# Kernel tuning notes

Measured on AMD Instinct MI355X. Metric: run time of the kernel, lower is better.

The kernel has to match this reference:

```python
import jax, jax.numpy as jnp
import numpy as np

B, L, P, NH = 16384, 64, 2, 128
T = L // P          # number of patches (GRU steps)
NOUT = 1 << P       # softmax over 2**p possible patches


def setup_inputs() -> dict:
    key = jax.random.key(0)
    ks = jax.random.split(key, 10)
    s_in = 1.0 / np.sqrt(NH)
    x = jax.random.randint(ks[0], (B, L, 1), 0, 2).astype(jnp.float32)
    return {
        "x": x,
        # GRU params, torch layout: gates ordered (r, z, n)
        "w_ih": jax.random.normal(ks[1], (3 * NH, P), jnp.float32) * s_in,
        "w_hh": jax.random.normal(ks[2], (3 * NH, NH), jnp.float32) * s_in,
        "b_ih": jax.random.normal(ks[3], (3 * NH,), jnp.float32) * s_in,
        "b_hh": jax.random.normal(ks[4], (3 * NH,), jnp.float32) * s_in,
        # MLP head: Linear(Nh,Nh) -> ReLU -> Linear(Nh, 2**p) -> Softmax
        "w1": jax.random.normal(ks[5], (NH, NH), jnp.float32) * s_in,
        "b1": jax.random.normal(ks[6], (NH,), jnp.float32) * s_in,
        "w2": jax.random.normal(ks[7], (NOUT, NH), jnp.float32) * s_in,
        "b2": jax.random.normal(ks[8], (NOUT,), jnp.float32) * s_in,
    }


def _gru_mlp_logp(x, w_ih, w_hh, b_ih, b_hh, w1, b1, w2, b2):
    b = x.shape[0]
    patches = x.reshape(b, T, P)                       # Patch1D.forward
    # shift right by one patch (teacher forcing input), first step is zeros
    data = jnp.concatenate([jnp.zeros((b, 1, P), x.dtype), patches[:, :-1]], axis=1)
    # precompute all input-side gate projections: [B,T,3*Nh]
    xi = jnp.einsum('btp,gp->btg', data, w_ih) + b_ih

    def step(h, xi_t):
        gi_r, gi_z, gi_n = jnp.split(xi_t, 3, axis=-1)
        gh = h @ w_hh.T + b_hh
        gh_r, gh_z, gh_n = jnp.split(gh, 3, axis=-1)
        r = jax.nn.sigmoid(gi_r + gh_r)
        z = jax.nn.sigmoid(gi_z + gh_z)
        n = jnp.tanh(gi_n + r * gh_n)
        h_new = (1.0 - z) * n + z * h
        return h_new, h_new

    h0 = jnp.zeros((b, NH), x.dtype)
    _, hs = jax.lax.scan(step, h0, jnp.swapaxes(xi, 0, 1))  # [T,B,Nh]
    hs = jnp.swapaxes(hs, 0, 1)                              # [B,T,Nh]

    hid = jax.nn.relu(hs @ w1.T + b1)
    probs = jax.nn.softmax(hid @ w2.T + b2, axis=-1)         # [B,T,2**p]

    # genpatch2onehot: binary-encode each patch, little-endian (bit i -> 2**i)
    weights = (1 << jnp.arange(P)).astype(jnp.float32)
    idx = jnp.sum(patches * weights, axis=-1).astype(jnp.int32)  # [B,T]
    total = jnp.take_along_axis(probs, idx[..., None], axis=-1)[..., 0]
    return jnp.sum(jnp.log(total), axis=1)                   # [B]


def reference(x, w_ih, w_hh, b_ih, b_hh, w1, b1, w2, b2):
    return _gru_mlp_logp(x, w_ih, w_hh, b_ih, b_hh, w1, b1, w2, b2)
```

## Files before the change

kernel.cpp:

```cpp
#include <hip/hip_runtime.h>
#include <hip/hip_bf16.h>


#define NSTEP 32
#define BT    32
#define BLK   256

using s8v = __attribute__((ext_vector_type(8))) short;
using f4v = __attribute__((ext_vector_type(4))) float;

#define L2E 1.4426950408889634f
#define LN2 0.6931471805599453f

__device__ __forceinline__ unsigned short f2bf(float f) {
  __hip_bfloat16 h = __float2bfloat16(f);
  return __builtin_bit_cast(unsigned short, h);
}
__device__ __forceinline__ unsigned pkbf2(float a, float b) {
  return (unsigned)f2bf(a) | ((unsigned)f2bf(b) << 16);
}
__device__ __forceinline__ s8v pack8(float4 u, float4 v) {
  s8v a;
  a[0]=(short)f2bf(u.x); a[1]=(short)f2bf(u.y); a[2]=(short)f2bf(u.z); a[3]=(short)f2bf(u.w);
  a[4]=(short)f2bf(v.x); a[5]=(short)f2bf(v.y); a[6]=(short)f2bf(v.z); a[7]=(short)f2bf(v.w);
  return a;
}
__device__ __forceinline__ f4v mfma16(s8v a, s8v b, f4v c) {
  return __builtin_amdgcn_mfma_f32_16x16x32_bf16(a, b, c, 0, 0, 0);
}
__device__ __forceinline__ float sigm(float x) {
  return __builtin_amdgcn_rcpf(1.f + __builtin_amdgcn_exp2f(-L2E * x));
}
__device__ __forceinline__ float tanhc(float x) {
  return __builtin_fmaf(2.f, __builtin_amdgcn_rcpf(1.f + __builtin_amdgcn_exp2f((-2.f*L2E) * x)), -1.f);
}

__global__ __launch_bounds__(BLK, 2) void prnn_kernel(
    const float* __restrict__ x, const float* __restrict__ w_ih,
    const float* __restrict__ w_hh, const float* __restrict__ b_ih,
    const float* __restrict__ b_hh, const float* __restrict__ w1,
    const float* __restrict__ b1, const float* __restrict__ w2,
    const float* __restrict__ b2, float* __restrict__ out) {

  __shared__ __align__(16) unsigned char lds_whhn[8*4*64*16];
  __shared__ __align__(16) unsigned char lds_h[4*2*64*16];
  __shared__ __align__(16) unsigned char lds_hid[2*4*2*64*16];
  __shared__ __align__(16) unsigned char lds_w2f[4*64*16];
  __shared__ __align__(16) float lds_xrz[64*4*4];
  __shared__ __align__(16) float lds_xn[32*4*4];
  __shared__ unsigned lds_idx[32*8];
  __shared__ float lds_lp[4][32];

  const int tid = threadIdx.x;
  const int bbase = blockIdx.x * BT;
  const int lane = tid & 63;
  const int lg = lane >> 4, ln = lane & 15;
  const int js = __builtin_amdgcn_readfirstlane(tid >> 6);

  {
    int b = tid >> 3, ch = tid & 7;
    const float* xp = x + (size_t)(bbase + b) * 64 + ch * 8;
    float4 v0 = *(const float4*)xp, v1 = *(const float4*)(xp + 4);
    unsigned pk = ((v0.x!=0.f?1u:0u) | (v0.y!=0.f?2u:0u))
               | (((v0.z!=0.f?1u:0u) | (v0.w!=0.f?2u:0u)) << 8)
               | (((v1.x!=0.f?1u:0u) | (v1.y!=0.f?2u:0u)) << 16)
               | (((v1.z!=0.f?1u:0u) | (v1.w!=0.f?2u:0u)) << 24);
    lds_idx[b*8 + ch] = pk;
  }
  {
    int j = tid;
    float base = b_ih[j] + b_hh[j];
    float wa = w_ih[2*j], wb = w_ih[2*j+1];
    int q = j >> 2, e = j & 3;
    #pragma unroll
    for (int v = 0; v < 4; ++v)
      lds_xrz[(q*4+v)*4 + e] = base + ((v&1) ? wa : 0.f) + ((v&2) ? wb : 0.f);
    if (tid < 128) {
      int j2 = 256 + tid;
      float bn = b_ih[j2];
      float wan = w_ih[2*j2], wbn = w_ih[2*j2+1];
      int qn = tid >> 2, en = tid & 3;
      #pragma unroll
      for (int v = 0; v < 4; ++v)
        lds_xn[(qn*4+v)*4 + en] = bn + ((v&1) ? wan : 0.f) + ((v&2) ? wbn : 0.f);
    }
  }
  #pragma unroll
  for (int it = 0; it < 8; ++it) {
    int i = tid + it * 256;
    int mt = i >> 8, ks = (i >> 6) & 3, l = i & 63;
    int lgg = l >> 4, lnn = l & 15;
    const float* src = w_hh + (256 + 16*mt + lnn) * 128 + ks*32 + lgg*8;
    s8v fr = pack8(*(const float4*)src, *(const float4*)(src + 4));
    *(s8v*)(lds_whhn + ((mt*4 + ks)*64 + l) * 16) = fr;
  }
  {
    int ks = tid >> 6, l = tid & 63;
    int lgg = l >> 4, lnn = l & 15;
    s8v fr;
    #pragma unroll
    for (int e = 0; e < 8; ++e) fr[e] = (short)0;
    if (lnn < 4) {
      const float* src = w2 + lnn * 128 + ks*32 + lgg*8;
      fr = pack8(*(const float4*)src, *(const float4*)(src + 4));
    }
    *(s8v*)(lds_w2f + (ks*64 + l) * 16) = fr;
  }

  s8v Ar[2][4], Az[2][4], wA1[2][4];
  f4v bhn2[2], b1f[2], b2r;
  #pragma unroll
  for (int p = 0; p < 2; ++p) {
    int row = 32*js + 16*p + ln;
    #pragma unroll
    for (int ks = 0; ks < 4; ++ks) {
      const float* s0 = w_hh + row * 128 + ks*32 + lg*8;
      Ar[p][ks] = pack8(*(const float4*)s0, *(const float4*)(s0 + 4));
      const float* s1 = w_hh + (128 + row) * 128 + ks*32 + lg*8;
      Az[p][ks] = pack8(*(const float4*)s1, *(const float4*)(s1 + 4));
      const float* s2 = w1 + row * 128 + ks*32 + lg*8;
      wA1[p][ks] = pack8(*(const float4*)s2, *(const float4*)(s2 + 4));
    }
    int jr = 32*js + 16*p + 4*lg;
    bhn2[p] = *(const f4v*)(b_hh + 256 + jr);
    b1f[p]  = *(const f4v*)(b1 + jr);
  }
  if (lg == 0) b2r = *(const f4v*)b2;
  else { b2r[0]=0.f; b2r[1]=0.f; b2r[2]=0.f; b2r[3]=0.f; }

  __syncthreads();

  unsigned pk0a=0, pk0b=0, pk1a=0, pk1b=0;
  #pragma unroll
  for (int w8 = 0; w8 < 4; ++w8) {
    unsigned u = lds_idx[ln*8 + w8];
    pk0a |= (((u&3u) | ((u>>6)&0xCu) | ((u>>12)&0x30u) | ((u>>18)&0xC0u)) << (8*w8));
    unsigned u2 = lds_idx[(16+ln)*8 + w8];
    pk1a |= (((u2&3u) | ((u2>>6)&0xCu) | ((u2>>12)&0x30u) | ((u2>>18)&0xC0u)) << (8*w8));
  }
  #pragma unroll
  for (int w8 = 4; w8 < 8; ++w8) {
    unsigned u = lds_idx[ln*8 + w8];
    pk0b |= (((u&3u) | ((u>>6)&0xCu) | ((u>>12)&0x30u) | ((u>>18)&0xC0u)) << (8*(w8-4)));
    unsigned u2 = lds_idx[(16+ln)*8 + w8];
    pk1b |= (((u2&3u) | ((u2>>6)&0xCu) | ((u2>>12)&0x30u) | ((u2>>18)&0xC0u)) << (8*(w8-4)));
  }

  const f4v* XRZ = (const f4v*)lds_xrz;
  const f4v* XN  = (const f4v*)lds_xn;

  s8v Bf[4][2];
  #pragma unroll
  for (int ks = 0; ks < 4; ++ks)
    #pragma unroll
    for (int nt = 0; nt < 2; ++nt)
      #pragma unroll
      for (int e = 0; e < 8; ++e) Bf[ks][nt][e] = (short)0;
  f4v hfr[2][2];
  #pragma unroll
  for (int p = 0; p < 2; ++p)
    #pragma unroll
    for (int nt = 0; nt < 2; ++nt) { hfr[p][nt][0]=0.f; hfr[p][nt][1]=0.f; hfr[p][nt][2]=0.f; hfr[p][nt][3]=0.f; }
  float lp0 = 0.f, lp1 = 0.f;
  int pv0 = 0, pv1 = 0;

  for (int tb = 0; tb < NSTEP; tb += 4) {
    #pragma unroll
    for (int k = 0; k < 4; ++k) {
      const int t = tb + k;
      uint2 hwv[2][2];
      #pragma unroll
      for (int nt = 0; nt < 2; ++nt) {
        const int var = nt ? pv1 : pv0;
        f4v aR[2], aZ[2], aN[2], xnv[2];
        #pragma unroll
        for (int p = 0; p < 2; ++p) {
          const int q = 8*js + 4*p + lg;
          aR[p]  = XRZ[(q     )*4 + var];
          aZ[p]  = XRZ[(q + 32)*4 + var];
          xnv[p] = XN [(q     )*4 + var];
          aN[p]  = bhn2[p];
        }
        #pragma unroll
        for (int ks = 0; ks < 4; ++ks) {
          s8v An0 = *(const s8v*)(lds_whhn + (((2*js+0)*4 + ks)*64 + lane)*16);
          s8v An1 = *(const s8v*)(lds_whhn + (((2*js+1)*4 + ks)*64 + lane)*16);
          aR[0] = mfma16(Ar[0][ks], Bf[ks][nt], aR[0]);
          aR[1] = mfma16(Ar[1][ks], Bf[ks][nt], aR[1]);
          aZ[0] = mfma16(Az[0][ks], Bf[ks][nt], aZ[0]);
          aZ[1] = mfma16(Az[1][ks], Bf[ks][nt], aZ[1]);
          aN[0] = mfma16(An0,       Bf[ks][nt], aN[0]);
          aN[1] = mfma16(An1,       Bf[ks][nt], aN[1]);
        }
        #pragma unroll
        for (int p = 0; p < 2; ++p) {
          f4v hn;
          #pragma unroll
          for (int r = 0; r < 4; ++r) {
            float R  = sigm(aR[p][r]);
            float Z  = sigm(aZ[p][r]);
            float Ng = tanhc(__builtin_fmaf(R, aN[p][r], xnv[p][r]));
            hn[r] = __builtin_fmaf(Z, hfr[p][nt][r] - Ng, Ng);
          }
          hfr[p][nt] = hn;
          hwv[p][nt].x = pkbf2(hn[0], hn[1]);
          hwv[p][nt].y = pkbf2(hn[2], hn[3]);
        }
      }
      #pragma unroll
      for (int p = 0; p < 2; ++p) {
        const int lgp = (2*p + (lg >> 1)) & 3;
        #pragma unroll
        for (int nt = 0; nt < 2; ++nt)
          *(uint2*)(lds_h + (((js*2 + nt)*64) + lgp*16 + ln)*16 + 8*(lg & 1)) = hwv[p][nt];
      }
      __syncthreads();
      #pragma unroll
      for (int ks = 0; ks < 4; ++ks)
        #pragma unroll
        for (int nt = 0; nt < 2; ++nt)
          Bf[ks][nt] = *(const s8v*)(lds_h + ((ks*2 + nt)*64 + lane)*16);
      f4v hc[2][2];
      #pragma unroll
      for (int p = 0; p < 2; ++p) { hc[p][0] = b1f[p]; hc[p][1] = b1f[p]; }
      #pragma unroll
      for (int ks = 0; ks < 4; ++ks)
        #pragma unroll
        for (int p = 0; p < 2; ++p) {
          hc[p][0] = mfma16(wA1[p][ks], Bf[ks][0], hc[p][0]);
          hc[p][1] = mfma16(wA1[p][ks], Bf[ks][1], hc[p][1]);
        }
      #pragma unroll
      for (int p = 0; p < 2; ++p) {
        const int lgp = (2*p + (lg >> 1)) & 3;
        #pragma unroll
        for (int nt = 0; nt < 2; ++nt) {
          uint2 wv;
          wv.x = pkbf2(fmaxf(hc[p][nt][0], 0.f), fmaxf(hc[p][nt][1], 0.f));
          wv.y = pkbf2(fmaxf(hc[p][nt][2], 0.f), fmaxf(hc[p][nt][3], 0.f));
          *(uint2*)(lds_hid + (k&1)*8192 + ((js*2 + nt)*64 + lgp*16 + ln)*16 + 8*(lg & 1)) = wv;
        }
      }
      __syncthreads();
      const unsigned pc0 = (t & 16) ? pk0b : pk0a;
      const unsigned pc1 = (t & 16) ? pk1b : pk1a;
      const int sh  = (2*t) & 31;
      const int ic0 = (pc0 >> sh) & 3;
      const int ic1 = (pc1 >> sh) & 3;
      if (js == k) {
        f4v la0 = b2r, la1 = b2r;
        #pragma unroll
        for (int ks = 0; ks < 4; ++ks) {
          s8v W2f = *(const s8v*)(lds_w2f + (ks*64 + lane)*16);
          s8v Bh0 = *(const s8v*)(lds_hid + (k&1)*8192 + ((ks*2 + 0)*64 + lane)*16);
          s8v Bh1 = *(const s8v*)(lds_hid + (k&1)*8192 + ((ks*2 + 1)*64 + lane)*16);
          la0 = mfma16(W2f, Bh0, la0);
          la1 = mfma16(W2f, Bh1, la1);
        }
        if (lg == 0) {
          {
            float l0=la0[0], l1=la0[1], l2=la0[2], l3=la0[3];
            float m = fmaxf(fmaxf(l0, l1), fmaxf(l2, l3));
            float s = __builtin_amdgcn_exp2f((l0-m)*L2E) + __builtin_amdgcn_exp2f((l1-m)*L2E)
                    + __builtin_amdgcn_exp2f((l2-m)*L2E) + __builtin_amdgcn_exp2f((l3-m)*L2E);
            float sel = (ic0 == 0) ? l0 : (ic0 == 1) ? l1 : (ic0 == 2) ? l2 : l3;
            lp0 += (sel - m) - __builtin_amdgcn_logf(s) * LN2;
          }
          {
            float l0=la1[0], l1=la1[1], l2=la1[2], l3=la1[3];
            float m = fmaxf(fmaxf(l0, l1), fmaxf(l2, l3));
            float s = __builtin_amdgcn_exp2f((l0-m)*L2E) + __builtin_amdgcn_exp2f((l1-m)*L2E)
                    + __builtin_amdgcn_exp2f((l2-m)*L2E) + __builtin_amdgcn_exp2f((l3-m)*L2E);
            float sel = (ic1 == 0) ? l0 : (ic1 == 1) ? l1 : (ic1 == 2) ? l2 : l3;
            lp1 += (sel - m) - __builtin_amdgcn_logf(s) * LN2;
          }
        }
      }
      pv0 = ic0; pv1 = ic1;
    }
  }

  if (lg == 0) { lds_lp[js][ln] = lp0; lds_lp[js][16 + ln] = lp1; }
  __syncthreads();
  if (tid < 32) {
    float s = lds_lp[0][tid] + lds_lp[1][tid] + lds_lp[2][tid] + lds_lp[3][tid];
    out[bbase + tid] = s;
  }
}

extern "C" void kernel_launch(void* const* d_in, const int* in_sizes, int n_in,
                              void* d_out, int out_size, void* d_ws, size_t ws_size,
                              hipStream_t stream) {
  const float* x    = (const float*)d_in[0];
  const float* w_ih = (const float*)d_in[1];
  const float* w_hh = (const float*)d_in[2];
  const float* b_ih = (const float*)d_in[3];
  const float* b_hh = (const float*)d_in[4];
  const float* w1   = (const float*)d_in[5];
  const float* b1   = (const float*)d_in[6];
  const float* w2   = (const float*)d_in[7];
  const float* b2   = (const float*)d_in[8];
  float* out = (float*)d_out;
  int B = in_sizes[0] / 64;
  int grid = B / BT;
  prnn_kernel<<<grid, BLK, 0, stream>>>(x, w_ih, w_hh, b_ih, b_hh, w1, b1, w2, b2, out);
}
```

Before: 105.4 us.

## Split GRU hidden rows across eight waves and move W1 to LDS

```diff
diff --git a/kernel.cpp b/kernel.cpp
--- a/kernel.cpp
+++ b/kernel.cpp
@@ -4,7 +4,7 @@
 
 #define NSTEP 32
 #define BT    32
-#define BLK   256
+#define BLK   512
 
 using s8v = __attribute__((ext_vector_type(8))) short;
 using f4v = __attribute__((ext_vector_type(4))) float;
@@ -35,29 +35,31 @@
   return __builtin_fmaf(2.f, __builtin_amdgcn_rcpf(1.f + __builtin_amdgcn_exp2f((-2.f*L2E) * x)), -1.f);
 }
 
-__global__ __launch_bounds__(BLK, 2) void prnn_kernel(
+__global__ __launch_bounds__(BLK, 4) void prnn_kernel(
     const float* __restrict__ x, const float* __restrict__ w_ih,
     const float* __restrict__ w_hh, const float* __restrict__ b_ih,
     const float* __restrict__ b_hh, const float* __restrict__ w1,
     const float* __restrict__ b1, const float* __restrict__ w2,
     const float* __restrict__ b2, float* __restrict__ out) {
 
-  __shared__ __align__(16) unsigned char lds_whhn[8*4*64*16];
   __shared__ __align__(16) unsigned char lds_h[4*2*64*16];
-  __shared__ __align__(16) unsigned char lds_hid[2*4*2*64*16];
+  __shared__ __align__(16) unsigned char lds_hid[4*2*64*16];
+  __shared__ __align__(16) unsigned char lds_wA1[8*4*64*16];
   __shared__ __align__(16) unsigned char lds_w2f[4*64*16];
   __shared__ __align__(16) float lds_xrz[64*4*4];
   __shared__ __align__(16) float lds_xn[32*4*4];
+  __shared__ __align__(16) float lds_bb[256];
+  __shared__ __align__(16) float lds_b2[4];
   __shared__ unsigned lds_idx[32*8];
-  __shared__ float lds_lp[4][32];
+  __shared__ float lds_lp[8][32];
 
   const int tid = threadIdx.x;
   const int bbase = blockIdx.x * BT;
   const int lane = tid & 63;
   const int lg = lane >> 4, ln = lane & 15;
-  const int js = __builtin_amdgcn_readfirstlane(tid >> 6);
-
-  {
+  const int w = __builtin_amdgcn_readfirstlane(tid >> 6);
+
+  if (tid < 256) {
     int b = tid >> 3, ch = tid & 7;
     const float* xp = x + (size_t)(bbase + b) * 64 + ch * 8;
     float4 v0 = *(const float4*)xp, v1 = *(const float4*)(xp + 4);
@@ -67,7 +69,7 @@
                | (((v1.z!=0.f?1u:0u) | (v1.w!=0.f?2u:0u)) << 24);
     lds_idx[b*8 + ch] = pk;
   }
-  {
+  if (tid < 256) {
     int j = tid;
     float base = b_ih[j] + b_hh[j];
     float wa = w_ih[2*j], wb = w_ih[2*j+1];
@@ -75,58 +77,51 @@
     #pragma unroll
     for (int v = 0; v < 4; ++v)
       lds_xrz[(q*4+v)*4 + e] = base + ((v&1) ? wa : 0.f) + ((v&2) ? wb : 0.f);
-    if (tid < 128) {
-      int j2 = 256 + tid;
-      float bn = b_ih[j2];
-      float wan = w_ih[2*j2], wbn = w_ih[2*j2+1];
-      int qn = tid >> 2, en = tid & 3;
-      #pragma unroll
-      for (int v = 0; v < 4; ++v)
-        lds_xn[(qn*4+v)*4 + en] = bn + ((v&1) ? wan : 0.f) + ((v&2) ? wbn : 0.f);
-    }
-  }
-  #pragma unroll
-  for (int it = 0; it < 8; ++it) {
-    int i = tid + it * 256;
+  }
+  if (tid < 128) {
+    int j2 = 256 + tid;
+    float bn = b_ih[j2];
+    float wan = w_ih[2*j2], wbn = w_ih[2*j2+1];
+    int qn = tid >> 2, en = tid & 3;
+    #pragma unroll
+    for (int v = 0; v < 4; ++v)
+      lds_xn[(qn*4+v)*4 + en] = bn + ((v&1) ? wan : 0.f) + ((v&2) ? wbn : 0.f);
+  }
+  if (tid < 128) lds_bb[tid] = b_hh[256 + tid];
+  else if (tid < 256) lds_bb[tid] = b1[tid - 128];
+  if (tid < 4) lds_b2[tid] = b2[tid];
+  #pragma unroll
+  for (int it = 0; it < 4; ++it) {
+    int i = tid + it * BLK;
     int mt = i >> 8, ks = (i >> 6) & 3, l = i & 63;
-    int lgg = l >> 4, lnn = l & 15;
-    const float* src = w_hh + (256 + 16*mt + lnn) * 128 + ks*32 + lgg*8;
-    s8v fr = pack8(*(const float4*)src, *(const float4*)(src + 4));
-    *(s8v*)(lds_whhn + ((mt*4 + ks)*64 + l) * 16) = fr;
-  }
-  {
+    const float* src = w1 + (16*mt + (l & 15)) * 128 + ks*32 + (l >> 4)*8;
+    *(s8v*)(lds_wA1 + ((mt*4 + ks)*64 + l)*16) = pack8(*(const float4*)src, *(const float4*)(src+4));
+  }
+  if (tid < 256) {
     int ks = tid >> 6, l = tid & 63;
-    int lgg = l >> 4, lnn = l & 15;
     s8v fr;
     #pragma unroll
     for (int e = 0; e < 8; ++e) fr[e] = (short)0;
-    if (lnn < 4) {
-      const float* src = w2 + lnn * 128 + ks*32 + lgg*8;
+    if ((l & 15) < 4) {
+      const float* src = w2 + (l & 15) * 128 + ks*32 + (l >> 4)*8;
       fr = pack8(*(const float4*)src, *(const float4*)(src + 4));
     }
-    *(s8v*)(lds_w2f + (ks*64 + l) * 16) = fr;
-  }
-
-  s8v Ar[2][4], Az[2][4], wA1[2][4];
-  f4v bhn2[2], b1f[2], b2r;
-  #pragma unroll
-  for (int p = 0; p < 2; ++p) {
-    int row = 32*js + 16*p + ln;
+    *(s8v*)(lds_w2f + (ks*64 + l)*16) = fr;
+  }
+
+  s8v Ar[4], Az[4], An[4];
+  {
+    const int row = 16*w + ln;
     #pragma unroll
     for (int ks = 0; ks < 4; ++ks) {
-      const float* s0 = w_hh + row * 128 + ks*32 + lg*8;
-      Ar[p][ks] = pack8(*(const float4*)s0, *(const float4*)(s0 + 4));
-      const float* s1 = w_hh + (128 + row) * 128 + ks*32 + lg*8;
-      Az[p][ks] = pack8(*(const float4*)s1, *(const float4*)(s1 + 4));
-      const float* s2 = w1 + row * 128 + ks*32 + lg*8;
-      wA1[p][ks] = pack8(*(const float4*)s2, *(const float4*)(s2 + 4));
+      const float* s0 = w_hh + row*128 + ks*32 + lg*8;
+      Ar[ks] = pack8(*(const float4*)s0, *(const float4*)(s0 + 4));
+      const float* s1 = s0 + 128*128;
+      Az[ks] = pack8(*(const float4*)s1, *(const float4*)(s1 + 4));
+      const float* s2 = s0 + 256*128;
+      An[ks] = pack8(*(const float4*)s2, *(const float4*)(s2 + 4));
     }
-    int jr = 32*js + 16*p + 4*lg;
-    bhn2[p] = *(const f4v*)(b_hh + 256 + jr);
-    b1f[p]  = *(const f4v*)(b1 + jr);
-  }
-  if (lg == 0) b2r = *(const f4v*)b2;
-  else { b2r[0]=0.f; b2r[1]=0.f; b2r[2]=0.f; b2r[3]=0.f; }
+  }
 
   __syncthreads();
 
@@ -146,8 +141,8 @@
     pk1b |= (((u2&3u) | ((u2>>6)&0xCu) | ((u2>>12)&0x30u) | ((u2>>18)&0xC0u)) << (8*(w8-4)));
   }
 
-  const f4v* XRZ = (const f4v*)lds_xrz;
-  const f4v* XN  = (const f4v*)lds_xn;
+  const unsigned wroff = (unsigned)((((w>>1)*128) + 16*(2*(w&1) + (lg>>1)) + ln)*16 + 8*(lg&1));
+  const int q = 4*w + lg;
 
   s8v Bf[4][2];
   #pragma unroll
@@ -156,63 +151,45 @@
     for (int nt = 0; nt < 2; ++nt)
       #pragma unroll
       for (int e = 0; e < 8; ++e) Bf[ks][nt][e] = (short)0;
-  f4v hfr[2][2];
-  #pragma unroll
-  for (int p = 0; p < 2; ++p)
-    #pragma unroll
-    for (int nt = 0; nt < 2; ++nt) { hfr[p][nt][0]=0.f; hfr[p][nt][1]=0.f; hfr[p][nt][2]=0.f; hfr[p][nt][3]=0.f; }
+  f4v hfr[2];
+  hfr[0][0]=0.f; hfr[0][1]=0.f; hfr[0][2]=0.f; hfr[0][3]=0.f;
+  hfr[1] = hfr[0];
   float lp0 = 0.f, lp1 = 0.f;
   int pv0 = 0, pv1 = 0;
 
-  for (int tb = 0; tb < NSTEP; tb += 4) {
-    #pragma unroll
-    for (int k = 0; k < 4; ++k) {
+  for (int tb = 0; tb < NSTEP; tb += 8) {
+    const unsigned pc0 = (tb & 16) ? pk0b : pk0a;
+    const unsigned pc1 = (tb & 16) ? pk1b : pk1a;
+    #pragma unroll
+    for (int k = 0; k < 8; ++k) {
       const int t = tb + k;
-      uint2 hwv[2][2];
+      const f4v aNi = *(const f4v*)&lds_bb[q*4];
       #pragma unroll
       for (int nt = 0; nt < 2; ++nt) {
         const int var = nt ? pv1 : pv0;
-        f4v aR[2], aZ[2], aN[2], xnv[2];
-        #pragma unroll
-        for (int p = 0; p < 2; ++p) {
-          const int q = 8*js + 4*p + lg;
-          aR[p]  = XRZ[(q     )*4 + var];
-          aZ[p]  = XRZ[(q + 32)*4 + var];
-          xnv[p] = XN [(q     )*4 + var];
-          aN[p]  = bhn2[p];
-        }
+        f4v aR = *(const f4v*)&lds_xrz[(q*4 + var)*4];
+        f4v aZ = *(const f4v*)&lds_xrz[((q+32)*4 + var)*4];
+        f4v aN = aNi;
         #pragma unroll
         for (int ks = 0; ks < 4; ++ks) {
-          s8v An0 = *(const s8v*)(lds_whhn + (((2*js+0)*4 + ks)*64 + lane)*16);
-          s8v An1 = *(const s8v*)(lds_whhn + (((2*js+1)*4 + ks)*64 + lane)*16);
-          aR[0] = mfma16(Ar[0][ks], Bf[ks][nt], aR[0]);
-          aR[1] = mfma16(Ar[1][ks], Bf[ks][nt], aR[1]);
-          aZ[0] = mfma16(Az[0][ks], Bf[ks][nt], aZ[0]);
-          aZ[1] = mfma16(Az[1][ks], Bf[ks][nt], aZ[1]);
-          aN[0] = mfma16(An0,       Bf[ks][nt], aN[0]);
-          aN[1] = mfma16(An1,       Bf[ks][nt], aN[1]);
-        }
-        #pragma unroll
-        for (int p = 0; p < 2; ++p) {
-          f4v hn;
-          #pragma unroll
-          for (int r = 0; r < 4; ++r) {
-            float R  = sigm(aR[p][r]);
-            float Z  = sigm(aZ[p][r]);
-            float Ng = tanhc(__builtin_fmaf(R, aN[p][r], xnv[p][r]));
-            hn[r] = __builtin_fmaf(Z, hfr[p][nt][r] - Ng, Ng);
-          }
-          hfr[p][nt] = hn;
-          hwv[p][nt].x = pkbf2(hn[0], hn[1]);
-          hwv[p][nt].y = pkbf2(hn[2], hn[3]);
-        }
-      }
-      #pragma unroll
-      for (int p = 0; p < 2; ++p) {
-        const int lgp = (2*p + (lg >> 1)) & 3;
-        #pragma unroll
-        for (int nt = 0; nt < 2; ++nt)
-          *(uint2*)(lds_h + (((js*2 + nt)*64) + lgp*16 + ln)*16 + 8*(lg & 1)) = hwv[p][nt];
+          aR = mfma16(Ar[ks], Bf[ks][nt], aR);
+          aZ = mfma16(Az[ks], Bf[ks][nt], aZ);
+          aN = mfma16(An[ks], Bf[ks][nt], aN);
+        }
+        const f4v xnv = *(const f4v*)&lds_xn[(q*4 + var)*4];
+        f4v hn;
+        #pragma unroll
+        for (int r = 0; r < 4; ++r) {
+          float R  = sigm(aR[r]);
+          float Z  = sigm(aZ[r]);
+          float Ng = tanhc(__builtin_fmaf(R, aN[r], xnv[r]));
+          hn[r] = __builtin_fmaf(Z, hfr[nt][r] - Ng, Ng);
+        }
+        hfr[nt] = hn;
+        uint2 wv;
+        wv.x = pkbf2(hn[0], hn[1]);
+        wv.y = pkbf2(hn[2], hn[3]);
+        *(uint2*)(lds_h + wroff + (unsigned)(nt*1024)) = wv;
       }
       __syncthreads();
       #pragma unroll
@@ -220,42 +197,40 @@
         #pragma unroll
         for (int nt = 0; nt < 2; ++nt)
           Bf[ks][nt] = *(const s8v*)(lds_h + ((ks*2 + nt)*64 + lane)*16);
-      f4v hc[2][2];
-      #pragma unroll
-      for (int p = 0; p < 2; ++p) { hc[p][0] = b1f[p]; hc[p][1] = b1f[p]; }
-      #pragma unroll
-      for (int ks = 0; ks < 4; ++ks)
-        #pragma unroll
-        for (int p = 0; p < 2; ++p) {
-          hc[p][0] = mfma16(wA1[p][ks], Bf[ks][0], hc[p][0]);
-          hc[p][1] = mfma16(wA1[p][ks], Bf[ks][1], hc[p][1]);
-        }
-      #pragma unroll
-      for (int p = 0; p < 2; ++p) {
-        const int lgp = (2*p + (lg >> 1)) & 3;
-        #pragma unroll
-        for (int nt = 0; nt < 2; ++nt) {
-          uint2 wv;
-          wv.x = pkbf2(fmaxf(hc[p][nt][0], 0.f), fmaxf(hc[p][nt][1], 0.f));
-          wv.y = pkbf2(fmaxf(hc[p][nt][2], 0.f), fmaxf(hc[p][nt][3], 0.f));
-          *(uint2*)(lds_hid + (k&1)*8192 + ((js*2 + nt)*64 + lgp*16 + ln)*16 + 8*(lg & 1)) = wv;
-        }
+      const f4v b1i = *(const f4v*)&lds_bb[128 + q*4];
+      f4v hc0 = b1i, hc1 = b1i;
+      #pragma unroll
+      for (int ks = 0; ks < 4; ++ks) {
+        const s8v wf = *(const s8v*)(lds_wA1 + ((w*4 + ks)*64 + lane)*16);
+        hc0 = mfma16(wf, Bf[ks][0], hc0);
+        hc1 = mfma16(wf, Bf[ks][1], hc1);
+      }
+      {
+        uint2 wv;
+        wv.x = pkbf2(fmaxf(hc0[0],0.f), fmaxf(hc0[1],0.f));
+        wv.y = pkbf2(fmaxf(hc0[2],0.f), fmaxf(hc0[3],0.f));
+        *(uint2*)(lds_hid + wroff) = wv;
+        wv.x = pkbf2(fmaxf(hc1[0],0.f), fmaxf(hc1[1],0.f));
+        wv.y = pkbf2(fmaxf(hc1[2],0.f), fmaxf(hc1[3],0.f));
+        *(uint2*)(lds_hid + wroff + 1024u) = wv;
       }
       __syncthreads();
-      const unsigned pc0 = (t & 16) ? pk0b : pk0a;
-      const unsigned pc1 = (t & 16) ? pk1b : pk1a;
       const int sh  = (2*t) & 31;
-      const int ic0 = (pc0 >> sh) & 3;
-      const int ic1 = (pc1 >> sh) & 3;
-      if (js == k) {
-        f4v la0 = b2r, la1 = b2r;
+      const int ic0 = (int)((pc0 >> sh) & 3);
+      const int ic1 = (int)((pc1 >> sh) & 3);
+      if (w == k) {
+        const f4v b2v = *(const f4v*)lds_b2;
+        f4v la0, la1;
+        #pragma unroll
+        for (int r = 0; r < 4; ++r) {
+          la0[r] = (lg == 0) ? b2v[r] : 0.f;
+          la1[r] = la0[r];
+        }
         #pragma unroll
         for (int ks = 0; ks < 4; ++ks) {
-          s8v W2f = *(const s8v*)(lds_w2f + (ks*64 + lane)*16);
-          s8v Bh0 = *(const s8v*)(lds_hid + (k&1)*8192 + ((ks*2 + 0)*64 + lane)*16);
-          s8v Bh1 = *(const s8v*)(lds_hid + (k&1)*8192 + ((ks*2 + 1)*64 + lane)*16);
-          la0 = mfma16(W2f, Bh0, la0);
-          la1 = mfma16(W2f, Bh1, la1);
+          const s8v W2f = *(const s8v*)(lds_w2f + (ks*64 + lane)*16);
+          la0 = mfma16(W2f, *(const s8v*)(lds_hid + ((ks*2 + 0)*64 + lane)*16), la0);
+          la1 = mfma16(W2f, *(const s8v*)(lds_hid + ((ks*2 + 1)*64 + lane)*16), la1);
         }
         if (lg == 0) {
           {
@@ -280,10 +255,12 @@
     }
   }
 
-  if (lg == 0) { lds_lp[js][ln] = lp0; lds_lp[js][16 + ln] = lp1; }
+  if (lg == 0) { lds_lp[w][ln] = lp0; lds_lp[w][16 + ln] = lp1; }
   __syncthreads();
   if (tid < 32) {
-    float s = lds_lp[0][tid] + lds_lp[1][tid] + lds_lp[2][tid] + lds_lp[3][tid];
+    float s = 0.f;
+    #pragma unroll
+    for (int ww = 0; ww < 8; ++ww) s += lds_lp[ww][tid];
     out[bbase + tid] = s;
   }
 }
```

Measured after the change: 100.0 us. 5.1% less time.
